# Performance work log

Hardware: AMD Instinct MI355X
Metric: run time of the kernel (lower is better)

The kernel has to match this reference:

```python
import jax, jax.numpy as jnp
import numpy as np

B, N = 4, 2048
EXPR, TIME, POSF = 512, 128, 128
H, HD = 8, 64
D = EXPR  # total_features_out_dim == d_model == 512
TOTAL_IN = EXPR + TIME + POSF  # 768
EPS_RMS = 1e-6


def _lin(key, fan_in, fan_out):
    kw, kb = jax.random.split(key)
    lim = 1.0 / np.sqrt(fan_in)
    W = jax.random.uniform(kw, (fan_in, fan_out), minval=-lim, maxval=lim, dtype=jnp.float32)
    b = jax.random.uniform(kb, (fan_out,), minval=-lim, maxval=lim, dtype=jnp.float32)
    return W, b


def setup_inputs() -> dict:
    key = jax.random.key(0)
    ks = jax.random.split(key, 20)
    inp = {}
    inp["expression_features"] = jax.random.normal(ks[0], (B, N, EXPR), dtype=jnp.float32)
    inp["diffusion_time"] = jax.random.normal(ks[1], (B, TIME), dtype=jnp.float32)
    inp["position_features"] = jax.random.normal(ks[2], (B, N, 3), dtype=jnp.float32)
    # position MLP: 4 -> 64 -> POSF
    inp["pos_w1"], inp["pos_b1"] = _lin(ks[3], 4, 64)
    inp["pos_w2"], inp["pos_b2"] = _lin(ks[4], 64, POSF)
    # expression MLP: EXPR -> 64 -> EXPR
    inp["expr_w1"], inp["expr_b1"] = _lin(ks[5], EXPR, 64)
    inp["expr_w2"], inp["expr_b2"] = _lin(ks[6], 64, EXPR)
    # time transform
    inp["yy_w"], inp["yy_b"] = _lin(ks[7], TIME, TIME)
    # concatenated features linear: TOTAL_IN -> D
    inp["cat_w"], inp["cat_b"] = _lin(ks[8], TOTAL_IN, D)
    # attention projections (headwise gating: q_proj outputs D + H)
    inp["q_w"], inp["q_b"] = _lin(ks[9], D, D + H)
    inp["k_w"], inp["k_b"] = _lin(ks[10], D, D)
    inp["v_w"], inp["v_b"] = _lin(ks[11], D, D)
    inp["o_w"], inp["o_b"] = _lin(ks[12], D, D)
    inp["qn_w"] = jnp.ones((HD,), dtype=jnp.float32)
    inp["kn_w"] = jnp.ones((HD,), dtype=jnp.float32)
    # output heads
    inp["hp_w"], inp["hp_b"] = _lin(ks[13], D, 3)
    inp["he_w"], inp["he_b"] = _lin(ks[14], D, EXPR)
    return inp


def _rmsnorm(x, w):
    xf = x.astype(jnp.float32)
    var = jnp.mean(xf * xf, axis=-1, keepdims=True)
    return (w * (xf * jax.lax.rsqrt(var + EPS_RMS))).astype(x.dtype)


def reference(expression_features, diffusion_time, position_features,
              pos_w1, pos_b1, pos_w2, pos_b2,
              expr_w1, expr_b1, expr_w2, expr_b2,
              yy_w, yy_b, cat_w, cat_b,
              q_w, q_b, k_w, k_b, v_w, v_b, o_w, o_b,
              qn_w, kn_w, hp_w, hp_b, he_w, he_b):
    b, n, _ = expression_features.shape
    # expression MLP
    te = jax.nn.relu(expression_features @ expr_w1 + expr_b1) @ expr_w2 + expr_b2
    # position features: direction + norm -> MLP
    nrm = jnp.linalg.norm(position_features, axis=-1, keepdims=True)
    direction = position_features / (nrm + 1e-7)
    pfeat = jnp.concatenate([direction, nrm], axis=-1)  # (B,N,4)
    tp = jax.nn.relu(pfeat @ pos_w1 + pos_b1) @ pos_w2 + pos_b2
    # diffusion time transform (not last layer)
    tdt = diffusion_time @ yy_w + yy_b  # (B,TIME)
    time_exp = jnp.broadcast_to(tdt[:, None, :], (b, n, tdt.shape[-1]))
    cat = jnp.concatenate([te, time_exp, tp], axis=-1)  # (B,N,TOTAL_IN)
    h = cat @ cat_w + cat_b  # (B,N,D)
    # gated multi-head attention
    qfull = h @ q_w + q_b  # (B,N,D+H)
    Q, gate = qfull[..., :D], qfull[..., D:]  # (B,N,D), (B,N,H)
    K = h @ k_w + k_b
    V = h @ v_w + v_b
    Q = Q.reshape(b, n, H, HD).transpose(0, 2, 1, 3)  # (B,H,N,hd)
    K = K.reshape(b, n, H, HD).transpose(0, 2, 1, 3)
    V = V.reshape(b, n, H, HD).transpose(0, 2, 1, 3)
    Q = _rmsnorm(Q, qn_w)
    K = _rmsnorm(K, kn_w)
    scores = jnp.einsum('bhqd,bhkd->bhqk', Q, K) / np.sqrt(HD)
    attn = jax.nn.softmax(scores.astype(jnp.float32), axis=-1).astype(Q.dtype)
    ao = jnp.einsum('bhqk,bhkd->bhqd', attn, V)  # (B,H,N,hd)
    ao = ao.transpose(0, 2, 1, 3)  # (B,N,H,hd)
    ao = ao * jax.nn.sigmoid(gate)[..., None]  # headwise gating
    ao = ao.reshape(b, n, D)
    out = ao @ o_w + o_b  # (B,N,D)
    expr_out = out @ he_w + he_b  # (B,N,EXPR)
    pos_out = out @ hp_w + hp_b   # (B,N,3)
    return expr_out, pos_out, tdt
```

## Files before the change

### kernel.cpp

```cpp
#include <hip/hip_runtime.h>
#include <math.h>

#define SEQ   2048
#define NROWS 8192

typedef unsigned short ushort_t;
typedef __attribute__((ext_vector_type(8))) short bf16x8;
typedef __attribute__((ext_vector_type(4))) float f32x4;

#define U_EXPR   0ull
#define U_A192   4194304ull
#define U_H      5767168ull
#define U_QKV    9961472ull
#define U_KN     26804224ull
#define U_VT     30998528ull
#define U_AO     35192832ull
#define U_W1T    39387136ull
#define U_W2RAW  39419904ull
#define U_CATWT  39452672ull
#define U_QKVWT  39845888ull
#define U_HEWT   40898560ull
#define U_WPRIME 41160704ull
#define U_WOHE   41259008ull
#define U_F32    41521152ull
#define U_ORAW   41537536ull

#define F_TDT    0
#define F_QKVB   512
#define F_BIASH  2056
#define F_BIASEO 4104
#define F_BIASPO 4616
#define F_WHP    4620

#define DOUT_EXPR 0ull
#define DOUT_POS  4194304ull
#define DOUT_TDT  4218880ull

#define LOG2E 1.44269504088896340736f

static __device__ __forceinline__ ushort_t f2bf(float f) {
    union { float f; unsigned int u; } v; v.f = f;
    unsigned int r = (v.u + 0x7fffu + ((v.u >> 16) & 1u)) >> 16;
    return (ushort_t)r;
}
static __device__ __forceinline__ float bf2f(ushort_t u) {
    union { unsigned int u; float f; } v; v.u = ((unsigned int)u) << 16;
    return v.f;
}

static __device__ __forceinline__ void gload16(const void* g, void* l) {
    __builtin_amdgcn_global_load_lds(
        (const __attribute__((address_space(1))) void*)g,
        (__attribute__((address_space(3))) void*)l,
        16, 0, 0);
}

template <int RELU, int OUT_BF16, int HASBIAS, int BBSTRIDE>
static __device__ void hgemm_body(
    const ushort_t* __restrict__ A, int lda,
    const ushort_t* __restrict__ Wt, int ldw,
    const float* __restrict__ bias,
    void* __restrict__ Cv, int ldc,
    int N, int K, int bx, int by,
    ushort_t* AsB, ushort_t* BsB)
{
    const int tid = threadIdx.x;
    const int lane = tid & 63, w = tid >> 6;
    const int lo = lane & 15, hi = lane >> 4;
    const int wm = w >> 2, wn = w & 3;
    const long m0 = (long)by * 128;
    const int n0 = bx * 128;

    f32x4 acc[4][2];
#pragma unroll
    for (int mt = 0; mt < 4; ++mt)
#pragma unroll
        for (int nt = 0; nt < 2; ++nt) acc[mt][nt] = (f32x4)0.f;

    auto stage = [&](int kt, int buf) {
#pragma unroll
        for (int i = 0; i < 2; ++i) {
            int c = w * 128 + i * 64 + lane;
            int r = c >> 3, ch = c & 7;
            int sch = ch ^ (r & 7);
            gload16(&A[(m0 + r) * (long)lda + kt + sch * 8],
                    &AsB[buf * 8192 + (w * 128 + i * 64) * 8]);
            gload16(&Wt[(long)(n0 + r) * ldw + kt + sch * 8],
                    &BsB[buf * 8192 + (w * 128 + i * 64) * 8]);
        }
    };

    stage(0, 0);
    __syncthreads();

    int cur = 0;
    for (int kt = 0; kt < K; kt += 64) {
        if (kt + 64 < K) stage(kt + 64, cur ^ 1);

#pragma unroll
        for (int ks = 0; ks < 2; ++ks) {
            bf16x8 af[4], bfr[2];
#pragma unroll
            for (int mt = 0; mt < 4; ++mt) {
                int m = wm * 64 + mt * 16 + lo;
                af[mt] = *(const bf16x8*)&AsB[cur * 8192 + m * 64 +
                                              (((ks * 4 + hi) ^ (lo & 7)) * 8)];
            }
#pragma unroll
            for (int nt = 0; nt < 2; ++nt) {
                int n = wn * 32 + nt * 16 + lo;
                bfr[nt] = *(const bf16x8*)&BsB[cur * 8192 + n * 64 +
                                               (((ks * 4 + hi) ^ (lo & 7)) * 8)];
            }
#pragma unroll
            for (int mt = 0; mt < 4; ++mt)
#pragma unroll
                for (int nt = 0; nt < 2; ++nt)
                    acc[mt][nt] = __builtin_amdgcn_mfma_f32_16x16x32_bf16(
                        af[mt], bfr[nt], acc[mt][nt], 0, 0, 0);
        }
        __syncthreads();
        cur ^= 1;
    }

#pragma unroll
    for (int mt = 0; mt < 4; ++mt)
#pragma unroll
        for (int nt = 0; nt < 2; ++nt) {
            int col = n0 + wn * 32 + nt * 16 + lo;
            if (col < N) {
                float bv = 0.f;
                if (HASBIAS)
                    bv = BBSTRIDE ? bias[(int)(m0 >> 11) * BBSTRIDE + col] : bias[col];
#pragma unroll
                for (int r = 0; r < 4; ++r) {
                    long row = m0 + wm * 64 + mt * 16 + hi * 4 + r;
                    float v = acc[mt][nt][r] + bv;
                    if (RELU) v = fmaxf(v, 0.f);
                    if (OUT_BF16) ((ushort_t*)Cv)[row * (long)ldc + col] = f2bf(v);
                    else          ((float*)Cv)[row * (long)ldc + col] = v;
                }
            }
        }
}

template <int RELU, int OUT_BF16, int HASBIAS, int BBSTRIDE>
__global__ __launch_bounds__(512) void hgemm(
    const ushort_t* __restrict__ A, int lda,
    const ushort_t* __restrict__ Wt, int ldw,
    const float* __restrict__ bias,
    void* __restrict__ Cv, int ldc, int N, int K)
{
    __shared__ __align__(16) ushort_t ls[32768];
    hgemm_body<RELU, OUT_BF16, HASBIAS, BBSTRIDE>(
        A, lda, Wt, ldw, bias, Cv, ldc, N, K,
        blockIdx.x, blockIdx.y, ls, ls + 16384);
}

struct WtSeg { const float* src; ushort_t* dst; int K, N, tK, tile0, dstStride, mode; };
struct WtTable { WtSeg s[10]; };

__global__ __launch_bounds__(256) void wt_transpose(
    WtTable tab, const float* __restrict__ qb, const float* __restrict__ kb,
    const float* __restrict__ vb, float* __restrict__ bias_dst,
    const float* __restrict__ dt, const float* __restrict__ yyw,
    const float* __restrict__ yyb, float* __restrict__ tdt_ws,
    float* __restrict__ out_tail)
{
    const int bid = blockIdx.x;
    const int tid = threadIdx.x;
    if (bid == 665) {
        for (int t = tid; t < 512; t += 256) {
            int b = t >> 7, o = t & 127;
            float s = yyb[o];
            for (int k = 0; k < 128; ++k)
                s = fmaf(dt[b * 128 + k], yyw[k * 128 + o], s);
            tdt_ws[t] = s;
            out_tail[t] = s;
        }
        return;
    }
    if (bid >= 658) {
        int t = (bid - 658) * 256 + tid;
        if (t < 520) bias_dst[t] = qb[t];
        else if (t < 1032) bias_dst[t] = kb[t - 520];
        else if (t < 1544) bias_dst[t] = vb[t - 1032];
        return;
    }
    int si = 0;
#pragma unroll
    for (int i = 1; i < 10; ++i)
        if (bid >= tab.s[i].tile0) si = i;
    const WtSeg sg = tab.s[si];
    const int local = bid - sg.tile0;

    if (sg.mode == 1) {
        long base = (long)local * 16384;
#pragma unroll
        for (int i = 0; i < 8; ++i) {
            long p = base + i * 2048 + tid * 8;
            float4 a = *(const float4*)&sg.src[p];
            float4 b = *(const float4*)&sg.src[p + 4];
            bf16x8 o;
            o[0] = (short)f2bf(a.x); o[1] = (short)f2bf(a.y);
            o[2] = (short)f2bf(a.z); o[3] = (short)f2bf(a.w);
            o[4] = (short)f2bf(b.x); o[5] = (short)f2bf(b.y);
            o[6] = (short)f2bf(b.z); o[7] = (short)f2bf(b.w);
            *(bf16x8*)&sg.dst[p] = o;
        }
        return;
    }

    __shared__ float t[64][65];
    const int k0 = (local % sg.tK) * 64;
    const int n0 = (local / sg.tK) * 64;
#pragma unroll
    for (int i = 0; i < 16; ++i) {
        int e = tid + i * 256;
        int r = e >> 6, c = e & 63;
        float v = 0.f;
        if (k0 + r < sg.K && n0 + c < sg.N)
            v = sg.src[(long)(k0 + r) * sg.N + n0 + c];
        t[r][c] = v;
    }
    __syncthreads();
#pragma unroll
    for (int i = 0; i < 16; ++i) {
        int e = tid + i * 256;
        int rn = e >> 6, ck = e & 63;
        if (n0 + rn < sg.N && k0 + ck < sg.K)
            sg.dst[(long)(n0 + rn) * sg.dstStride + k0 + ck] = f2bf(t[ck][rn]);
    }
}

__global__ __launch_bounds__(512) void prep2_kernel(
    const ushort_t* __restrict__ catwt, const ushort_t* __restrict__ hewt,
    const ushort_t* __restrict__ w2raw, const ushort_t* __restrict__ o_raw,
    ushort_t* __restrict__ wprime, ushort_t* __restrict__ wohe,
    const float* __restrict__ expr_b2, const float* __restrict__ tdt,
    const float* __restrict__ cat_b, const float* __restrict__ o_b,
    const float* __restrict__ he_b, const float* __restrict__ o_w,
    const float* __restrict__ hp_w, const float* __restrict__ hp_b,
    float* __restrict__ bias_h, float* __restrict__ bias_eo,
    float* __restrict__ whp, float* __restrict__ bias_po)
{
    __shared__ __align__(16) ushort_t ls[32768];
    const int bid = blockIdx.x;
    const int tid = threadIdx.x;

    if (bid < 4) {
        hgemm_body<0, 1, 0, 0>(catwt, 768, w2raw, 512, nullptr, wprime, 192,
                               64, 512, 0, bid, ls, ls + 16384);
        return;
    }
    if (bid < 20) {
        int local = bid - 4;
        hgemm_body<0, 1, 0, 0>(hewt, 512, o_raw, 512, nullptr, wohe, 512,
                               512, 512, local & 3, local >> 2, ls, ls + 16384);
        return;
    }

    const int wid = (bid - 20) * 8 + (tid >> 6);
    const int lane = tid & 63;
    float s = 0.f;
    if (wid < 2048) {
        int b = wid >> 9, n = wid & 511;
        bf16x8 wv = *(const bf16x8*)&catwt[(long)n * 768 + lane * 8];
        float4 e0 = *(const float4*)&expr_b2[lane * 8];
        float4 e1 = *(const float4*)&expr_b2[lane * 8 + 4];
        s = bf2f((ushort_t)wv[0]) * e0.x + bf2f((ushort_t)wv[1]) * e0.y +
            bf2f((ushort_t)wv[2]) * e0.z + bf2f((ushort_t)wv[3]) * e0.w +
            bf2f((ushort_t)wv[4]) * e1.x + bf2f((ushort_t)wv[5]) * e1.y +
            bf2f((ushort_t)wv[6]) * e1.z + bf2f((ushort_t)wv[7]) * e1.w;
        float2 tt = *(const float2*)&tdt[b * 128 + lane * 2];
        s += bf2f(catwt[(long)n * 768 + 512 + lane * 2]) * tt.x;
        s += bf2f(catwt[(long)n * 768 + 513 + lane * 2]) * tt.y;
#pragma unroll
        for (int o = 32; o >= 1; o >>= 1) s += __shfl_xor(s, o);
        if (lane == 0) bias_h[b * 512 + n] = s + cat_b[n];
    } else if (wid < 2560) {
        int n = wid - 2048;
        bf16x8 wv = *(const bf16x8*)&hewt[(long)n * 512 + lane * 8];
        float4 e0 = *(const float4*)&o_b[lane * 8];
        float4 e1 = *(const float4*)&o_b[lane * 8 + 4];
        s = bf2f((ushort_t)wv[0]) * e0.x + bf2f((ushort_t)wv[1]) * e0.y +
            bf2f((ushort_t)wv[2]) * e0.z + bf2f((ushort_t)wv[3]) * e0.w +
            bf2f((ushort_t)wv[4]) * e1.x + bf2f((ushort_t)wv[5]) * e1.y +
            bf2f((ushort_t)wv[6]) * e1.z + bf2f((ushort_t)wv[7]) * e1.w;
#pragma unroll
        for (int o = 32; o >= 1; o >>= 1) s += __shfl_xor(s, o);
        if (lane == 0) bias_eo[n] = s + he_b[n];
    } else if (wid < 4096) {
        int t = wid - 2560;
        int c = t >> 9, k = t & 511;
#pragma unroll
        for (int i = 0; i < 8; ++i) {
            int j = i * 64 + lane;
            s = fmaf(o_w[(long)k * 512 + j], hp_w[j * 3 + c], s);
        }
#pragma unroll
        for (int o = 32; o >= 1; o >>= 1) s += __shfl_xor(s, o);
        if (lane == 0) whp[k * 3 + c] = s;
    } else if (wid < 4099) {
        int c = wid - 4096;
#pragma unroll
        for (int i = 0; i < 8; ++i) {
            int j = i * 64 + lane;
            s = fmaf(o_b[j], hp_w[j * 3 + c], s);
        }
#pragma unroll
        for (int o = 32; o >= 1; o >>= 1) s += __shfl_xor(s, o);
        if (lane == 0) bias_po[c] = s + hp_b[c];
    }
}

__global__ __launch_bounds__(512) void mlp_kernel(
    const ushort_t* __restrict__ expr_bf, const ushort_t* __restrict__ w1t,
    const float* __restrict__ expr_b1,
    const float* __restrict__ pos,
    const float* __restrict__ w1, const float* __restrict__ b1,
    const float* __restrict__ w2, const float* __restrict__ b2,
    ushort_t* __restrict__ a192)
{
    __shared__ __align__(16) ushort_t ls[32768];
    const int bid = blockIdx.x;
    const int tid = threadIdx.x;

    if (bid < 64) {
        hgemm_body<1, 1, 1, 0>(expr_bf, 512, w1t, 512, expr_b1, a192, 192,
                               64, 512, 0, bid, ls, ls + 16384);
        return;
    }

    float* w1s = (float*)ls;
    float* b1s = w1s + 256;
    float* b2s = b1s + 64;
    float* w2t = b2s + 128;
    if (tid < 256) w1s[tid] = w1[tid];
    if (tid >= 256 && tid < 320) b1s[tid - 256] = b1[tid - 256];
    if (tid >= 320 && tid < 448) b2s[tid - 320] = b2[tid - 320];
    for (int i = tid; i < 8192; i += 512) {
        int k = i >> 7, o = i & 127;
        w2t[o * 72 + k] = w2[i];
    }
    __syncthreads();

    const long r = (long)(bid - 64) * 64 + (tid >> 3);
    const int chunk = tid & 7;
    float px = pos[r * 3 + 0], py = pos[r * 3 + 1], pz = pos[r * 3 + 2];
    float nrm = sqrtf(px * px + py * py + pz * pz);
    float inv = 1.f / (nrm + 1e-7f);
    float pf0 = px * inv, pf1 = py * inv, pf2 = pz * inv, pf3 = nrm;

    float h1[64];
#pragma unroll
    for (int o = 0; o < 64; ++o) {
        float a = b1s[o];
        a = fmaf(pf0, w1s[o], a);
        a = fmaf(pf1, w1s[64 + o], a);
        a = fmaf(pf2, w1s[128 + o], a);
        a = fmaf(pf3, w1s[192 + o], a);
        h1[o] = fmaxf(a, 0.f);
    }
    ushort_t* dst = &a192[r * 192 + 64];
#pragma unroll
    for (int j = 0; j < 16; ++j) {
        int o = chunk + 8 * j;
        float s = b2s[o];
#pragma unroll
        for (int i4 = 0; i4 < 16; ++i4) {
            float4 wv = *(const float4*)&w2t[o * 72 + i4 * 4];
            s = fmaf(h1[i4 * 4 + 0], wv.x, s);
            s = fmaf(h1[i4 * 4 + 1], wv.y, s);
            s = fmaf(h1[i4 * 4 + 2], wv.z, s);
            s = fmaf(h1[i4 * 4 + 3], wv.w, s);
        }
        dst[o] = f2bf(s);
    }
}

__global__ __launch_bounds__(256) void qkvpost_kernel(
    const ushort_t* __restrict__ qkv, const float* __restrict__ knw,
    ushort_t* __restrict__ kn, ushort_t* __restrict__ Vt)
{
    __shared__ ushort_t t[64][72];
    __shared__ float knw_s[64];
    const int bh = blockIdx.x, b = bh >> 3, h = bh & 7;
    const int n0 = blockIdx.y * 64;
    const int tid = threadIdx.x;
    if (tid < 64) knw_s[tid] = knw[tid];
#pragma unroll
    for (int i = 0; i < 2; ++i) {
        int c = tid + i * 256;
        int r = c >> 3, ch = c & 7;
        *(bf16x8*)&t[r][ch * 8] =
            *(const bf16x8*)&qkv[(long)(b * SEQ + n0 + r) * 1544 + 1032 + h * 64 + ch * 8];
    }
    __syncthreads();
#pragma unroll
    for (int i = 0; i < 2; ++i) {
        int c = tid + i * 256;
        int r = c >> 3, ch = c & 7;
        bf16x8 kv = *(const bf16x8*)&qkv[(long)(b * SEQ + n0 + r) * 1544 + 520 + h * 64 + ch * 8];
        float x[8], ss = 0.f;
#pragma unroll
        for (int j = 0; j < 8; ++j) { x[j] = bf2f((ushort_t)kv[j]); ss = fmaf(x[j], x[j], ss); }
        ss += __shfl_xor(ss, 1);
        ss += __shfl_xor(ss, 2);
        ss += __shfl_xor(ss, 4);
        float invr = rsqrtf(ss * (1.f / 64.f) + 1e-6f);
        bf16x8 o;
#pragma unroll
        for (int j = 0; j < 8; ++j) o[j] = (short)f2bf(x[j] * knw_s[ch * 8 + j] * invr);
        *(bf16x8*)&kn[(long)(b * SEQ + n0 + r) * 512 + h * 64 + ch * 8] = o;
    }
    const int d = tid >> 2;
#pragma unroll
    for (int i = 0; i < 2; ++i) {
        int cc = (tid & 3) * 2 + i;
        bf16x8 pk;
#pragma unroll
        for (int j = 0; j < 8; ++j) pk[j] = (short)t[cc * 8 + j][d];
        *(bf16x8*)&Vt[((long)(bh * 64 + d)) * SEQ + n0 + cc * 8] = pk;
    }
}

__global__ __launch_bounds__(256) void flash_attn_mfma(
    const ushort_t* __restrict__ QKV, const ushort_t* __restrict__ Kn,
    const ushort_t* __restrict__ Vt, const float* __restrict__ qnw,
    ushort_t* __restrict__ AO)
{
    __shared__ __align__(16) ushort_t Ks[2][64 * 64];
    __shared__ __align__(16) ushort_t Vs[2][64 * 64];
    __shared__ __align__(16) ushort_t Ps[4][32 * 64];

    const int tid = threadIdx.x;
    const int lane = tid & 63;
    const int w = tid >> 6;
    const int lo = lane & 15, hi = lane >> 4;
    const int bh = blockIdx.x, b = bh >> 3, h = bh & 7;
    const int qb = blockIdx.y * 128 + w * 32;

    bf16x8 qfrag[2][2];
    {
        float qw[2][8];
#pragma unroll
        for (int ks = 0; ks < 2; ++ks)
#pragma unroll
            for (int j = 0; j < 8; ++j)
                qw[ks][j] = qnw[ks * 32 + hi * 8 + j];
#pragma unroll
        for (int jt = 0; jt < 2; ++jt) {
            float qx[2][8], ss = 0.f;
#pragma unroll
            for (int ks = 0; ks < 2; ++ks) {
                bf16x8 q = *(const bf16x8*)&QKV[(long)(b * SEQ + qb + jt * 16 + lo) * 1544 +
                                                h * 64 + ks * 32 + hi * 8];
#pragma unroll
                for (int j = 0; j < 8; ++j) {
                    qx[ks][j] = bf2f((ushort_t)q[j]);
                    ss = fmaf(qx[ks][j], qx[ks][j], ss);
                }
            }
            ss += __shfl_xor(ss, 16);
            ss += __shfl_xor(ss, 32);
            float invr = rsqrtf(ss * (1.f / 64.f) + 1e-6f) * (0.125f * LOG2E);
#pragma unroll
            for (int ks = 0; ks < 2; ++ks) {
                bf16x8 f;
#pragma unroll
                for (int j = 0; j < 8; ++j)
                    f[j] = (short)f2bf(qx[ks][j] * qw[ks][j] * invr);
                qfrag[jt][ks] = f;
            }
        }
    }

    f32x4 accO[2][4];
#pragma unroll
    for (int mt = 0; mt < 2; ++mt)
#pragma unroll
        for (int nt = 0; nt < 4; ++nt) accO[mt][nt] = (f32x4)0.f;
    float l_part[2] = {0.f, 0.f};

    const int sr0 = tid >> 3, sc0 = tid & 7;
    const int sr1 = (tid + 256) >> 3, sc1 = tid & 7;
    const int wo0 = sr0 * 64 + ((sc0 ^ (sr0 & 7)) * 8);
    const int wo1 = sr1 * 64 + ((sc1 ^ (sr1 & 7)) * 8);

    bf16x8 kreg0, kreg1, vreg0, vreg1;
    kreg0 = *(const bf16x8*)&Kn[(b * SEQ + sr0) * 512 + h * 64 + sc0 * 8];
    vreg0 = *(const bf16x8*)&Vt[((long)(bh * 64 + sr0)) * SEQ + sc0 * 8];
    kreg1 = *(const bf16x8*)&Kn[(b * SEQ + sr1) * 512 + h * 64 + sc1 * 8];
    vreg1 = *(const bf16x8*)&Vt[((long)(bh * 64 + sr1)) * SEQ + sc1 * 8];
    *(bf16x8*)&Ks[0][wo0] = kreg0;
    *(bf16x8*)&Vs[0][wo0] = vreg0;
    *(bf16x8*)&Ks[0][wo1] = kreg1;
    *(bf16x8*)&Vs[0][wo1] = vreg1;
    kreg0 = *(const bf16x8*)&Kn[(b * SEQ + 64 + sr0) * 512 + h * 64 + sc0 * 8];
    vreg0 = *(const bf16x8*)&Vt[((long)(bh * 64 + sr0)) * SEQ + 64 + sc0 * 8];
    kreg1 = *(const bf16x8*)&Kn[(b * SEQ + 64 + sr1) * 512 + h * 64 + sc1 * 8];
    vreg1 = *(const bf16x8*)&Vt[((long)(bh * 64 + sr1)) * SEQ + 64 + sc1 * 8];
    __syncthreads();

    auto step = [&](int kt, int cur, int nxt) {
        if (kt + 1 < 32) {
            *(bf16x8*)&Ks[nxt][wo0] = kreg0;
            *(bf16x8*)&Vs[nxt][wo0] = vreg0;
            *(bf16x8*)&Ks[nxt][wo1] = kreg1;
            *(bf16x8*)&Vs[nxt][wo1] = vreg1;
        }
        if (kt + 2 < 32) {
            int nk = (kt + 2) * 64;
            kreg0 = *(const bf16x8*)&Kn[(b * SEQ + nk + sr0) * 512 + h * 64 + sc0 * 8];
            vreg0 = *(const bf16x8*)&Vt[((long)(bh * 64 + sr0)) * SEQ + nk + sc0 * 8];
            kreg1 = *(const bf16x8*)&Kn[(b * SEQ + nk + sr1) * 512 + h * 64 + sc1 * 8];
            vreg1 = *(const bf16x8*)&Vt[((long)(bh * 64 + sr1)) * SEQ + nk + sc1 * 8];
        }

        f32x4 accS[4][2];
#pragma unroll
        for (int it = 0; it < 4; ++it)
#pragma unroll
            for (int jt = 0; jt < 2; ++jt) accS[it][jt] = (f32x4)0.f;

#pragma unroll
        for (int it = 0; it < 4; ++it) {
            bf16x8 kf[2];
#pragma unroll
            for (int ks = 0; ks < 2; ++ks)
                kf[ks] = *(const bf16x8*)&Ks[cur][(it * 16 + lo) * 64 +
                                                 (((ks * 4 + hi) ^ (lo & 7)) * 8)];
#pragma unroll
            for (int jt = 0; jt < 2; ++jt)
#pragma unroll
                for (int ks = 0; ks < 2; ++ks)
                    accS[it][jt] = __builtin_amdgcn_mfma_f32_16x16x32_bf16(
                        kf[ks], qfrag[jt][ks], accS[it][jt], 0, 0, 0);
        }

#pragma unroll
        for (int it = 0; it < 4; ++it)
#pragma unroll
            for (int jt = 0; jt < 2; ++jt) {
                float p0, p1, p2, p3;
                asm("v_exp_f32 %0, %1" : "=v"(p0) : "v"(accS[it][jt][0]));
                asm("v_exp_f32 %0, %1" : "=v"(p1) : "v"(accS[it][jt][1]));
                asm("v_exp_f32 %0, %1" : "=v"(p2) : "v"(accS[it][jt][2]));
                asm("v_exp_f32 %0, %1" : "=v"(p3) : "v"(accS[it][jt][3]));
                l_part[jt] += (p0 + p1) + (p2 + p3);
                unsigned w0, w1;
                asm("v_cvt_pk_bf16_f32 %0, %1, %2" : "=v"(w0) : "v"(p0), "v"(p1));
                asm("v_cvt_pk_bf16_f32 %0, %1, %2" : "=v"(w1) : "v"(p2), "v"(p3));
                int q = jt * 16 + lo;
                int cch = it * 2 + (hi >> 1);
                int off = q * 64 + ((cch ^ (q & 7)) * 8) + (hi & 1) * 4;
                uint2 t; t.x = w0; t.y = w1;
                *(uint2*)&Ps[w][off] = t;
            }

#pragma unroll
        for (int kk = 0; kk < 2; ++kk) {
            bf16x8 pf[2];
#pragma unroll
            for (int mt = 0; mt < 2; ++mt)
                pf[mt] = *(const bf16x8*)&Ps[w][(mt * 16 + lo) * 64 +
                                               (((kk * 4 + hi) ^ (lo & 7)) * 8)];
#pragma unroll
            for (int nt = 0; nt < 4; ++nt) {
                bf16x8 vf = *(const bf16x8*)&Vs[cur][(nt * 16 + lo) * 64 +
                                                    (((kk * 4 + hi) ^ (lo & 7)) * 8)];
#pragma unroll
                for (int mt = 0; mt < 2; ++mt)
                    accO[mt][nt] = __builtin_amdgcn_mfma_f32_16x16x32_bf16(
                        pf[mt], vf, accO[mt][nt], 0, 0, 0);
            }
        }
        __syncthreads();
    };

    for (int kt = 0; kt < 32; kt += 2) {
        step(kt, 0, 1);
        step(kt + 1, 1, 0);
    }

#pragma unroll
    for (int jt = 0; jt < 2; ++jt) {
        l_part[jt] += __shfl_xor(l_part[jt], 16);
        l_part[jt] += __shfl_xor(l_part[jt], 32);
    }

#pragma unroll
    for (int mt = 0; mt < 2; ++mt)
#pragma unroll
        for (int r = 0; r < 4; ++r) {
            float lq = __shfl(l_part[mt], hi * 4 + r);
            int grow = b * SEQ + qb + mt * 16 + hi * 4 + r;
            float g = bf2f(QKV[(long)grow * 1544 + 512 + h]);
            g = 1.f / (1.f + __expf(-g));
            float sc = g / lq;
#pragma unroll
            for (int nt = 0; nt < 4; ++nt)
                AO[(long)grow * 512 + h * 64 + nt * 16 + lo] = f2bf(accO[mt][nt][r] * sc);
        }
}

__global__ __launch_bounds__(512) void out_kernel(
    const ushort_t* __restrict__ ao, const ushort_t* __restrict__ wohe,
    const float* __restrict__ bias_eo, float* __restrict__ eo,
    const float* __restrict__ whp, const float* __restrict__ bpo,
    float* __restrict__ po)
{
    __shared__ __align__(16) ushort_t ls[32768];
    const int bid = blockIdx.x;
    const int tid = threadIdx.x;

    if (bid < 256) {
        hgemm_body<0, 0, 1, 0>(ao, 512, wohe, 512, bias_eo, eo, 512,
                               512, 512, bid & 3, bid >> 2, ls, ls + 16384);
        return;
    }

    const int lane = tid & 63;
    const long row = (long)(bid - 256) * 8 + (tid >> 6);
    float p0 = 0.f, p1 = 0.f, p2 = 0.f;
#pragma unroll
    for (int it = 0; it < 8; ++it) {
        int k = it * 64 + lane;
        float x = bf2f(ao[row * 512 + k]);
        p0 = fmaf(x, whp[k * 3 + 0], p0);
        p1 = fmaf(x, whp[k * 3 + 1], p1);
        p2 = fmaf(x, whp[k * 3 + 2], p2);
    }
#pragma unroll
    for (int o = 32; o >= 1; o >>= 1) {
        p0 += __shfl_xor(p0, o);
        p1 += __shfl_xor(p1, o);
        p2 += __shfl_xor(p2, o);
    }
    if (lane == 0) {
        po[row * 3 + 0] = p0 + bpo[0];
        po[row * 3 + 1] = p1 + bpo[1];
        po[row * 3 + 2] = p2 + bpo[2];
    }
}

extern "C" void kernel_launch(void* const* d_in, const int* in_sizes, int n_in,
                              void* d_out, int out_size, void* d_ws, size_t ws_size,
                              hipStream_t stream)
{
    const float* expr    = (const float*)d_in[0];
    const float* dtime   = (const float*)d_in[1];
    const float* posf    = (const float*)d_in[2];
    const float* pos_w1  = (const float*)d_in[3];
    const float* pos_b1  = (const float*)d_in[4];
    const float* pos_w2  = (const float*)d_in[5];
    const float* pos_b2  = (const float*)d_in[6];
    const float* expr_w1 = (const float*)d_in[7];
    const float* expr_b1 = (const float*)d_in[8];
    const float* expr_w2 = (const float*)d_in[9];
    const float* expr_b2 = (const float*)d_in[10];
    const float* yy_w    = (const float*)d_in[11];
    const float* yy_b    = (const float*)d_in[12];
    const float* cat_w   = (const float*)d_in[13];
    const float* cat_b   = (const float*)d_in[14];
    const float* q_w     = (const float*)d_in[15];
    const float* q_b     = (const float*)d_in[16];
    const float* k_w     = (const float*)d_in[17];
    const float* k_b     = (const float*)d_in[18];
    const float* v_w     = (const float*)d_in[19];
    const float* v_b     = (const float*)d_in[20];
    const float* o_w     = (const float*)d_in[21];
    const float* o_b     = (const float*)d_in[22];
    const float* qn_w    = (const float*)d_in[23];
    const float* kn_w    = (const float*)d_in[24];
    const float* hp_w    = (const float*)d_in[25];
    const float* hp_b    = (const float*)d_in[26];
    const float* he_w    = (const float*)d_in[27];
    const float* he_b    = (const float*)d_in[28];
    (void)in_sizes; (void)n_in; (void)out_size; (void)ws_size;

    ushort_t* wsb     = (ushort_t*)d_ws;
    ushort_t* expr_bf = wsb + U_EXPR;
    ushort_t* a192    = wsb + U_A192;
    ushort_t* h_bf    = wsb + U_H;
    ushort_t* qkv_bf  = wsb + U_QKV;
    ushort_t* kn_bf   = wsb + U_KN;
    ushort_t* vt_bf   = wsb + U_VT;
    ushort_t* ao_bf   = wsb + U_AO;
    ushort_t* w1t     = wsb + U_W1T;
    ushort_t* w2raw   = wsb + U_W2RAW;
    ushort_t* cat_wt  = wsb + U_CATWT;
    ushort_t* qkv_wt  = wsb + U_QKVWT;
    ushort_t* he_wt   = wsb + U_HEWT;
    ushort_t* wprime  = wsb + U_WPRIME;
    ushort_t* wohe    = wsb + U_WOHE;
    ushort_t* o_raw   = wsb + U_ORAW;
    float* f32r       = (float*)(wsb + U_F32);
    float* tdt        = f32r + F_TDT;
    float* qkv_bias   = f32r + F_QKVB;
    float* bias_h     = f32r + F_BIASH;
    float* bias_eo    = f32r + F_BIASEO;
    float* bias_po    = f32r + F_BIASPO;
    float* whp        = f32r + F_WHP;
    float* dout       = (float*)d_out;

    const dim3 blk(256);
    const dim3 blk512(512);

    WtTable tab;
    tab.s[0] = { expr_w1,          w1t,             512,  64,  8,   0, 512, 0 };
    tab.s[1] = { cat_w,            cat_wt,          768, 512, 12,   8, 768, 0 };
    tab.s[2] = { q_w,              qkv_wt,          512, 520,  8, 104, 512, 0 };
    tab.s[3] = { k_w,              qkv_wt + 520*512,512, 512,  8, 176, 512, 0 };
    tab.s[4] = { v_w,              qkv_wt +1032*512,512, 512,  8, 240, 512, 0 };
    tab.s[5] = { he_w,             he_wt,           512, 512,  8, 304, 512, 0 };
    tab.s[6] = { cat_w + 640*512,  wprime + 64,     128, 512,  2, 368, 192, 0 };
    tab.s[7] = { expr_w2,          w2raw,             0,   0,  0, 384,   0, 1 };
    tab.s[8] = { o_w,              o_raw,             0,   0,  0, 386,   0, 1 };
    tab.s[9] = { expr,             expr_bf,           0,   0,  0, 402,   0, 1 };
    wt_transpose<<<dim3(666), blk, 0, stream>>>(tab, q_b, k_b, v_b, qkv_bias,
                                                dtime, yy_w, yy_b, tdt,
                                                dout + DOUT_TDT);

    prep2_kernel<<<dim3(533), blk512, 0, stream>>>(
        cat_wt, he_wt, w2raw, o_raw, wprime, wohe,
        expr_b2, tdt, cat_b, o_b, he_b, o_w, hp_w, hp_b,
        bias_h, bias_eo, whp, bias_po);

    mlp_kernel<<<dim3(192), blk512, 0, stream>>>(
        expr_bf, w1t, expr_b1, posf, pos_w1, pos_b1, pos_w2, pos_b2, a192);
    hgemm<0, 1, 1, 512><<<dim3(4, 64), blk512, 0, stream>>>(a192, 192, wprime, 192,
                                                            bias_h, h_bf, 512, 512, 192);
    hgemm<0, 1, 1, 0><<<dim3(13, 64), blk512, 0, stream>>>(h_bf, 512, qkv_wt, 512,
                                                           qkv_bias, qkv_bf, 1544, 1544, 512);
    qkvpost_kernel<<<dim3(32, 32), blk, 0, stream>>>(qkv_bf, kn_w, kn_bf, vt_bf);
    flash_attn_mfma<<<dim3(32, 16), blk, 0, stream>>>(qkv_bf, kn_bf, vt_bf, qn_w, ao_bf);
    out_kernel<<<dim3(1280), blk512, 0, stream>>>(
        ao_bf, wohe, bias_eo, dout + DOUT_EXPR, whp, bias_po, dout + DOUT_POS);
}
```

Measured before the change: 135.2 us.

## Merge prep2 and MLP kernels, swizzle GEMM block order, compile-time K loop

Merges the weight-preparation kernel and the MLP kernel into a single launch with 725 blocks, removing one kernel launch and letting the two independent workloads run at the same time. The standalone GEMM now uses a 1D grid with an XCD-aware block swizzle so that neighbouring tiles land on the same chiplet and share L2. The K dimension becomes a template parameter, so the k-loop is fully unrolled. The swizzle assumes the grid size is a multiple of 8 and that the remapped index still covers every tile, and unrolling increases code size.

```diff
diff --git a/kernel.cpp b/kernel.cpp
--- a/kernel.cpp
+++ b/kernel.cpp
@@ -55,13 +55,13 @@
         16, 0, 0);
 }
 
-template <int RELU, int OUT_BF16, int HASBIAS, int BBSTRIDE>
+template <int RELU, int OUT_BF16, int HASBIAS, int BBSTRIDE, int KC>
 static __device__ void hgemm_body(
     const ushort_t* __restrict__ A, int lda,
     const ushort_t* __restrict__ Wt, int ldw,
     const float* __restrict__ bias,
     void* __restrict__ Cv, int ldc,
-    int N, int K, int bx, int by,
+    int N, int bx, int by,
     ushort_t* AsB, ushort_t* BsB)
 {
     const int tid = threadIdx.x;
@@ -93,9 +93,10 @@
     stage(0, 0);
     __syncthreads();
 
-    int cur = 0;
-    for (int kt = 0; kt < K; kt += 64) {
-        if (kt + 64 < K) stage(kt + 64, cur ^ 1);
+#pragma unroll
+    for (int step = 0; step < KC / 64; ++step) {
+        const int cur = step & 1;
+        if ((step + 1) * 64 < KC) stage((step + 1) * 64, cur ^ 1);
 
 #pragma unroll
         for (int ks = 0; ks < 2; ++ks) {
@@ -120,7 +121,6 @@
                         af[mt], bfr[nt], acc[mt][nt], 0, 0, 0);
         }
         __syncthreads();
-        cur ^= 1;
     }
 
 #pragma unroll
@@ -144,17 +144,21 @@
         }
 }
 
-template <int RELU, int OUT_BF16, int HASBIAS, int BBSTRIDE>
+template <int RELU, int OUT_BF16, int HASBIAS, int BBSTRIDE, int KC>
 __global__ __launch_bounds__(512) void hgemm(
     const ushort_t* __restrict__ A, int lda,
     const ushort_t* __restrict__ Wt, int ldw,
     const float* __restrict__ bias,
-    void* __restrict__ Cv, int ldc, int N, int K)
+    void* __restrict__ Cv, int ldc, int N, int gx)
 {
     __shared__ __align__(16) ushort_t ls[32768];
-    hgemm_body<RELU, OUT_BF16, HASBIAS, BBSTRIDE>(
-        A, lda, Wt, ldw, bias, Cv, ldc, N, K,
-        blockIdx.x, blockIdx.y, ls, ls + 16384);
+    const int nwg = gridDim.x;
+    const int bid = blockIdx.x;
+    const int cpx = nwg >> 3;
+    const int swz = (bid & 7) * cpx + (bid >> 3);
+    hgemm_body<RELU, OUT_BF16, HASBIAS, BBSTRIDE, KC>(
+        A, lda, Wt, ldw, bias, Cv, ldc, N,
+        swz % gx, swz / gx, ls, ls + 16384);
 }
 
 struct WtSeg { const float* src; ushort_t* dst; int K, N, tK, tile0, dstStride, mode; };
@@ -233,7 +237,7 @@
     }
 }
 
-__global__ __launch_bounds__(512) void prep2_kernel(
+__global__ __launch_bounds__(512) void prep2mlp_kernel(
     const ushort_t* __restrict__ catwt, const ushort_t* __restrict__ hewt,
     const ushort_t* __restrict__ w2raw, const ushort_t* __restrict__ o_raw,
     ushort_t* __restrict__ wprime, ushort_t* __restrict__ wohe,
@@ -242,79 +246,7 @@
     const float* __restrict__ he_b, const float* __restrict__ o_w,
     const float* __restrict__ hp_w, const float* __restrict__ hp_b,
     float* __restrict__ bias_h, float* __restrict__ bias_eo,
-    float* __restrict__ whp, float* __restrict__ bias_po)
-{
-    __shared__ __align__(16) ushort_t ls[32768];
-    const int bid = blockIdx.x;
-    const int tid = threadIdx.x;
-
-    if (bid < 4) {
-        hgemm_body<0, 1, 0, 0>(catwt, 768, w2raw, 512, nullptr, wprime, 192,
-                               64, 512, 0, bid, ls, ls + 16384);
-        return;
-    }
-    if (bid < 20) {
-        int local = bid - 4;
-        hgemm_body<0, 1, 0, 0>(hewt, 512, o_raw, 512, nullptr, wohe, 512,
-                               512, 512, local & 3, local >> 2, ls, ls + 16384);
-        return;
-    }
-
-    const int wid = (bid - 20) * 8 + (tid >> 6);
-    const int lane = tid & 63;
-    float s = 0.f;
-    if (wid < 2048) {
-        int b = wid >> 9, n = wid & 511;
-        bf16x8 wv = *(const bf16x8*)&catwt[(long)n * 768 + lane * 8];
-        float4 e0 = *(const float4*)&expr_b2[lane * 8];
-        float4 e1 = *(const float4*)&expr_b2[lane * 8 + 4];
-        s = bf2f((ushort_t)wv[0]) * e0.x + bf2f((ushort_t)wv[1]) * e0.y +
-            bf2f((ushort_t)wv[2]) * e0.z + bf2f((ushort_t)wv[3]) * e0.w +
-            bf2f((ushort_t)wv[4]) * e1.x + bf2f((ushort_t)wv[5]) * e1.y +
-            bf2f((ushort_t)wv[6]) * e1.z + bf2f((ushort_t)wv[7]) * e1.w;
-        float2 tt = *(const float2*)&tdt[b * 128 + lane * 2];
-        s += bf2f(catwt[(long)n * 768 + 512 + lane * 2]) * tt.x;
-        s += bf2f(catwt[(long)n * 768 + 513 + lane * 2]) * tt.y;
-#pragma unroll
-        for (int o = 32; o >= 1; o >>= 1) s += __shfl_xor(s, o);
-        if (lane == 0) bias_h[b * 512 + n] = s + cat_b[n];
-    } else if (wid < 2560) {
-        int n = wid - 2048;
-        bf16x8 wv = *(const bf16x8*)&hewt[(long)n * 512 + lane * 8];
-        float4 e0 = *(const float4*)&o_b[lane * 8];
-        float4 e1 = *(const float4*)&o_b[lane * 8 + 4];
-        s = bf2f((ushort_t)wv[0]) * e0.x + bf2f((ushort_t)wv[1]) * e0.y +
-            bf2f((ushort_t)wv[2]) * e0.z + bf2f((ushort_t)wv[3]) * e0.w +
-            bf2f((ushort_t)wv[4]) * e1.x + bf2f((ushort_t)wv[5]) * e1.y +
-            bf2f((ushort_t)wv[6]) * e1.z + bf2f((ushort_t)wv[7]) * e1.w;
-#pragma unroll
-        for (int o = 32; o >= 1; o >>= 1) s += __shfl_xor(s, o);
-        if (lane == 0) bias_eo[n] = s + he_b[n];
-    } else if (wid < 4096) {
-        int t = wid - 2560;
-        int c = t >> 9, k = t & 511;
-#pragma unroll
-        for (int i = 0; i < 8; ++i) {
-            int j = i * 64 + lane;
-            s = fmaf(o_w[(long)k * 512 + j], hp_w[j * 3 + c], s);
-        }
-#pragma unroll
-        for (int o = 32; o >= 1; o >>= 1) s += __shfl_xor(s, o);
-        if (lane == 0) whp[k * 3 + c] = s;
-    } else if (wid < 4099) {
-        int c = wid - 4096;
-#pragma unroll
-        for (int i = 0; i < 8; ++i) {
-            int j = i * 64 + lane;
-            s = fmaf(o_b[j], hp_w[j * 3 + c], s);
-        }
-#pragma unroll
-        for (int o = 32; o >= 1; o >>= 1) s += __shfl_xor(s, o);
-        if (lane == 0) bias_po[c] = s + hp_b[c];
-    }
-}
-
-__global__ __launch_bounds__(512) void mlp_kernel(
+    float* __restrict__ whp, float* __restrict__ bias_po,
     const ushort_t* __restrict__ expr_bf, const ushort_t* __restrict__ w1t,
     const float* __restrict__ expr_b1,
     const float* __restrict__ pos,
@@ -326,9 +258,75 @@
     const int bid = blockIdx.x;
     const int tid = threadIdx.x;
 
-    if (bid < 64) {
-        hgemm_body<1, 1, 1, 0>(expr_bf, 512, w1t, 512, expr_b1, a192, 192,
-                               64, 512, 0, bid, ls, ls + 16384);
+    if (bid < 4) {
+        hgemm_body<0, 1, 0, 0, 512>(catwt, 768, w2raw, 512, nullptr, wprime, 192,
+                                    64, 0, bid, ls, ls + 16384);
+        return;
+    }
+    if (bid < 20) {
+        int local = bid - 4;
+        hgemm_body<0, 1, 0, 0, 512>(hewt, 512, o_raw, 512, nullptr, wohe, 512,
+                                    512, local & 3, local >> 2, ls, ls + 16384);
+        return;
+    }
+    if (bid < 533) {
+        const int wid = (bid - 20) * 8 + (tid >> 6);
+        const int lane = tid & 63;
+        float s = 0.f;
+        if (wid < 2048) {
+            int b = wid >> 9, n = wid & 511;
+            bf16x8 wv = *(const bf16x8*)&catwt[(long)n * 768 + lane * 8];
+            float4 e0 = *(const float4*)&expr_b2[lane * 8];
+            float4 e1 = *(const float4*)&expr_b2[lane * 8 + 4];
+            s = bf2f((ushort_t)wv[0]) * e0.x + bf2f((ushort_t)wv[1]) * e0.y +
+                bf2f((ushort_t)wv[2]) * e0.z + bf2f((ushort_t)wv[3]) * e0.w +
+                bf2f((ushort_t)wv[4]) * e1.x + bf2f((ushort_t)wv[5]) * e1.y +
+                bf2f((ushort_t)wv[6]) * e1.z + bf2f((ushort_t)wv[7]) * e1.w;
+            float2 tt = *(const float2*)&tdt[b * 128 + lane * 2];
+            s += bf2f(catwt[(long)n * 768 + 512 + lane * 2]) * tt.x;
+            s += bf2f(catwt[(long)n * 768 + 513 + lane * 2]) * tt.y;
+#pragma unroll
+            for (int o = 32; o >= 1; o >>= 1) s += __shfl_xor(s, o);
+            if (lane == 0) bias_h[b * 512 + n] = s + cat_b[n];
+        } else if (wid < 2560) {
+            int n = wid - 2048;
+            bf16x8 wv = *(const bf16x8*)&hewt[(long)n * 512 + lane * 8];
+            float4 e0 = *(const float4*)&o_b[lane * 8];
+            float4 e1 = *(const float4*)&o_b[lane * 8 + 4];
+            s = bf2f((ushort_t)wv[0]) * e0.x + bf2f((ushort_t)wv[1]) * e0.y +
+                bf2f((ushort_t)wv[2]) * e0.z + bf2f((ushort_t)wv[3]) * e0.w +
+                bf2f((ushort_t)wv[4]) * e1.x + bf2f((ushort_t)wv[5]) * e1.y +
+                bf2f((ushort_t)wv[6]) * e1.z + bf2f((ushort_t)wv[7]) * e1.w;
+#pragma unroll
+            for (int o = 32; o >= 1; o >>= 1) s += __shfl_xor(s, o);
+            if (lane == 0) bias_eo[n] = s + he_b[n];
+        } else if (wid < 4096) {
+            int t = wid - 2560;
+            int c = t >> 9, k = t & 511;
+#pragma unroll
+            for (int i = 0; i < 8; ++i) {
+                int j = i * 64 + lane;
+                s = fmaf(o_w[(long)k * 512 + j], hp_w[j * 3 + c], s);
+            }
+#pragma unroll
+            for (int o = 32; o >= 1; o >>= 1) s += __shfl_xor(s, o);
+            if (lane == 0) whp[k * 3 + c] = s;
+        } else if (wid < 4099) {
+            int c = wid - 4096;
+#pragma unroll
+            for (int i = 0; i < 8; ++i) {
+                int j = i * 64 + lane;
+                s = fmaf(o_b[j], hp_w[j * 3 + c], s);
+            }
+#pragma unroll
+            for (int o = 32; o >= 1; o >>= 1) s += __shfl_xor(s, o);
+            if (lane == 0) bias_po[c] = s + hp_b[c];
+        }
+        return;
+    }
+    if (bid < 597) {
+        hgemm_body<1, 1, 1, 0, 512>(expr_bf, 512, w1t, 512, expr_b1, a192, 192,
+                                    64, 0, bid - 533, ls, ls + 16384);
         return;
     }
 
@@ -345,7 +343,7 @@
     }
     __syncthreads();
 
-    const long r = (long)(bid - 64) * 64 + (tid >> 3);
+    const long r = (long)(bid - 597) * 64 + (tid >> 3);
     const int chunk = tid & 7;
     float px = pos[r * 3 + 0], py = pos[r * 3 + 1], pz = pos[r * 3 + 2];
     float nrm = sqrtf(px * px + py * py + pz * pz);
@@ -616,8 +614,8 @@
     const int tid = threadIdx.x;
 
     if (bid < 256) {
-        hgemm_body<0, 0, 1, 0>(ao, 512, wohe, 512, bias_eo, eo, 512,
-                               512, 512, bid & 3, bid >> 2, ls, ls + 16384);
+        hgemm_body<0, 0, 1, 0, 512>(ao, 512, wohe, 512, bias_eo, eo, 512,
+                                    512, bid & 3, bid >> 2, ls, ls + 16384);
         return;
     }
 
@@ -723,17 +721,16 @@
                                                 dtime, yy_w, yy_b, tdt,
                                                 dout + DOUT_TDT);
 
-    prep2_kernel<<<dim3(533), blk512, 0, stream>>>(
+    prep2mlp_kernel<<<dim3(725), blk512, 0, stream>>>(
         cat_wt, he_wt, w2raw, o_raw, wprime, wohe,
         expr_b2, tdt, cat_b, o_b, he_b, o_w, hp_w, hp_b,
-        bias_h, bias_eo, whp, bias_po);
-
-    mlp_kernel<<<dim3(192), blk512, 0, stream>>>(
+        bias_h, bias_eo, whp, bias_po,
         expr_bf, w1t, expr_b1, posf, pos_w1, pos_b1, pos_w2, pos_b2, a192);
-    hgemm<0, 1, 1, 512><<<dim3(4, 64), blk512, 0, stream>>>(a192, 192, wprime, 192,
-                                                            bias_h, h_bf, 512, 512, 192);
-    hgemm<0, 1, 1, 0><<<dim3(13, 64), blk512, 0, stream>>>(h_bf, 512, qkv_wt, 512,
-                                                           qkv_bias, qkv_bf, 1544, 1544, 512);
+
+    hgemm<0, 1, 1, 512, 192><<<dim3(256), blk512, 0, stream>>>(
+        a192, 192, wprime, 192, bias_h, h_bf, 512, 512, 4);
+    hgemm<0, 1, 1, 0, 512><<<dim3(832), blk512, 0, stream>>>(
+        h_bf, 512, qkv_wt, 512, qkv_bias, qkv_bf, 1544, 1544, 13);
     qkvpost_kernel<<<dim3(32, 32), blk, 0, stream>>>(qkv_bf, kn_w, kn_bf, vt_bf);
     flash_attn_mfma<<<dim3(32, 16), blk, 0, stream>>>(qkv_bf, kn_bf, vt_bf, qn_w, ao_bf);
     out_kernel<<<dim3(1280), blk512, 0, stream>>>(
```

After: 124.3 us. 1.09x faster.
